# Kernel optimization log

Measured on AMD Instinct MI355X. Metric: run time of the kernel, lower is better.

Reference implementation:

```python
import jax, jax.numpy as jnp
import numpy as np

PRIOR_HOURS = 48.0
INIT_TIME = 0.0
K = 13  # nr_ref_time_points (time_space)
L = 200  # time steps (axis_2)
D = 64   # features (axis_3)
B = 64

REF_TIME = jnp.asarray(np.linspace(INIT_TIME, PRIOR_HOURS, K).reshape(K, 1, 1), dtype=jnp.float32)


def setup_inputs() -> dict:
    key = jax.random.key(0)
    ks = jax.random.split(key, 9)
    X = jax.random.normal(ks[0], (B, L, D), dtype=jnp.float32)
    T = jax.random.uniform(ks[1], (B, L, D), dtype=jnp.float32) * PRIOR_HOURS
    M = (jax.random.uniform(ks[2], (B, L, D)) > 0.5).astype(jnp.float32)
    DT = jax.random.uniform(ks[3], (B, L, D), dtype=jnp.float32)
    # trainable weights (keras random_normal initializer, stddev=0.05)
    alpha = jax.random.normal(ks[4], (K, 1, 1), dtype=jnp.float32) * 0.05
    w_v = jax.random.normal(ks[5], (K, L, D), dtype=jnp.float32) * 0.05
    w_t = jax.random.normal(ks[6], (K, L, D, 4), dtype=jnp.float32) * 0.05
    b_v = jax.random.normal(ks[7], (K, 1, D), dtype=jnp.float32) * 0.05
    b_t = jax.random.normal(ks[8], (K, L, D, 1), dtype=jnp.float32) * 0.05
    return {"X": X, "T": T, "M": M, "DT": DT, "alpha": alpha,
            "w_v": w_v, "w_t": w_t, "b_v": b_v, "b_t": b_t}


def reference(X, T, M, DT, alpha, w_v, w_t, b_v, b_t):
    # broadcast inputs over the K reference time points: [B,1,L,D] -> [B,K,L,D]
    dist = jnp.abs(T[:, None, :, :] - REF_TIME)                 # [B,K,L,D]
    kernel = jnp.exp(-jax.nn.relu(alpha) * dist)                # [B,K,L,D]
    intensity = jax.nn.relu(X[:, None, :, :] * kernel)          # [B,K,L,D]
    shp = intensity.shape
    x = jnp.broadcast_to(X[:, None, :, :], shp)
    dt = jnp.broadcast_to(DT[:, None, :, :], shp)
    m = jnp.broadcast_to(M[:, None, :, :], shp)
    feat = jnp.stack([x, dt, intensity, m], axis=-1)            # [B,K,L,D,4]
    # stage 1: weighted reduce over the 4-feature axis (b_t broadcasts over it)
    lat = jax.nn.relu(jnp.sum(w_t * feat + b_t, axis=-1))       # [B,K,L,D]
    # stage 2: weighted reduce over the time-step axis L (b_v broadcasts over it)
    out = jax.nn.relu(jnp.sum(w_v * lat + b_v, axis=2))         # [B,K,D]
    return out
```

## Files before the change

### kernel.cpp

```cpp
#include <hip/hip_runtime.h>


#define NB 64
#define NK 13
#define NL 200
#define ND 64
#define ND4 16
#define GB 8
#define LC 2
#define NC (NL / LC)

__global__ __launch_bounds__(256) void alnn_stage1(
    const float* __restrict__ X, const float* __restrict__ T,
    const float* __restrict__ M, const float* __restrict__ DT,
    const float* __restrict__ alpha, const float* __restrict__ w_v,
    const float* __restrict__ w_t, const float* __restrict__ b_t,
    float4* __restrict__ part)
{
    const int bid = blockIdx.x;
    const int clo = bid & 7;
    const int g   = bid >> 3;
    const int bg  = g & 7;
    const int chi = g >> 3;
    const int c   = chi * 8 + clo;
    if (c >= NC) return;

    const int tid = threadIdx.x;
    const int dq  = tid & 15;
    const int b8  = (tid >> 4) & 7;
    const int ks  = tid >> 7;
    const int k0  = ks * 7;
    const int b   = (bg << 3) + b8;
    const int la  = c * LC;

    const float4* X4  = (const float4*)X;
    const float4* T4  = (const float4*)T;
    const float4* M4  = (const float4*)M;
    const float4* DT4 = (const float4*)DT;
    const float4* WT4 = (const float4*)w_t;
    const float4* BT4 = (const float4*)b_t;
    const float4* WV4 = (const float4*)w_v;

    float av[7], rv[7];
    #pragma unroll
    for (int i = 0; i < 7; ++i) {
        const int k = k0 + i;
        av[i] = (k < NK) ? fmaxf(alpha[k], 0.f) : 0.f;
        rv[i] = 4.f * (float)k;
    }

    float4 acc[7];
    #pragma unroll
    for (int i = 0; i < 7; ++i) acc[i] = make_float4(0.f, 0.f, 0.f, 0.f);

#define COMP(c_, wt, A) {                                                 \
        const float dist  = fabsf(t4.c_ - reft);                          \
        const float inten = fmaxf(x4.c_ * __expf(-a * dist), 0.f);        \
        const float sf = wt.x * x4.c_ + wt.y * dt4.c_ + wt.z * inten +    \
                         wt.w * m4.c_ + 4.f * bt4.c_;                     \
        A.c_ = fmaf(wv4.c_, fmaxf(sf, 0.f), A.c_);                        \
    }

    #pragma unroll
    for (int li = 0; li < LC; ++li) {
        const int l  = la + li;
        const int io = (b * NL + l) * ND4 + dq;
        const float4 x4  = X4[io];
        const float4 t4  = T4[io];
        const float4 m4  = M4[io];
        const float4 dt4 = DT4[io];
        #pragma unroll
        for (int i = 0; i < 7; ++i) {
            const int k = k0 + i;
            if (k < NK) {
                const int w0 = (k * NL + l) * ND + (dq << 2);
                const float4 wt0 = WT4[w0 + 0];
                const float4 wt1 = WT4[w0 + 1];
                const float4 wt2 = WT4[w0 + 2];
                const float4 wt3 = WT4[w0 + 3];
                const int   wq  = (k * NL + l) * ND4 + dq;
                const float4 bt4 = BT4[wq];
                const float4 wv4 = WV4[wq];
                const float a    = av[i];
                const float reft = rv[i];
                COMP(x, wt0, acc[i])
                COMP(y, wt1, acc[i])
                COMP(z, wt2, acc[i])
                COMP(w, wt3, acc[i])
            }
        }
    }
#undef COMP

    const int pb = ((c * NB + b) * NK + k0) * ND4 + dq;
    #pragma unroll
    for (int i = 0; i < 7; ++i)
        if (k0 + i < NK) part[pb + i * ND4] = acc[i];
}

__global__ __launch_bounds__(256) void alnn_stage2(
    const float4* __restrict__ part, const float* __restrict__ b_v,
    float4* __restrict__ out)
{
    const int g  = blockIdx.x * 256 + threadIdx.x;
    const int dq = g & 15;
    const int r  = g >> 4;
    const int q  = r & 3;
    const int bk = r >> 2;
    if (bk >= NB * NK) return;

    float4 s = make_float4(0.f, 0.f, 0.f, 0.f);
    #pragma unroll 5
    for (int i = 0; i < NC / 4; ++i) {
        const int c = q * (NC / 4) + i;
        const float4 p = part[(c * NB * NK + bk) * ND4 + dq];
        s.x += p.x; s.y += p.y; s.z += p.z; s.w += p.w;
    }
    s.x += __shfl_xor(s.x, 16); s.y += __shfl_xor(s.y, 16);
    s.z += __shfl_xor(s.z, 16); s.w += __shfl_xor(s.w, 16);
    s.x += __shfl_xor(s.x, 32); s.y += __shfl_xor(s.y, 32);
    s.z += __shfl_xor(s.z, 32); s.w += __shfl_xor(s.w, 32);

    if (q == 0) {
        const int k = bk % NK;
        const float4 bv = ((const float4*)b_v)[k * ND4 + dq];
        float4 o;
        o.x = fmaxf(s.x + 200.f * bv.x, 0.f);
        o.y = fmaxf(s.y + 200.f * bv.y, 0.f);
        o.z = fmaxf(s.z + 200.f * bv.z, 0.f);
        o.w = fmaxf(s.w + 200.f * bv.w, 0.f);
        out[bk * ND4 + dq] = o;
    }
}

extern "C" void kernel_launch(void* const* d_in, const int* in_sizes, int n_in,
                              void* d_out, int out_size, void* d_ws, size_t ws_size,
                              hipStream_t stream) {
    const float* X     = (const float*)d_in[0];
    const float* T     = (const float*)d_in[1];
    const float* M     = (const float*)d_in[2];
    const float* DT    = (const float*)d_in[3];
    const float* alpha = (const float*)d_in[4];
    const float* w_v   = (const float*)d_in[5];
    const float* w_t   = (const float*)d_in[6];
    const float* b_v   = (const float*)d_in[7];
    const float* b_t   = (const float*)d_in[8];

    float4* part = (float4*)d_ws;

    alnn_stage1<<<832, 256, 0, stream>>>(X, T, M, DT, alpha, w_v, w_t, b_t, part);
    alnn_stage2<<<(NB * NK * 64) / 256, 256, 0, stream>>>(part, b_v, (float4*)d_out);
}
```

Before: 101.4 us.

## Split L chunk across thread halves and pre-reduce partials with shuffles

Each stage-1 block now covers 4 time steps, with the two 16-lane halves of a 32-lane group each taking two. The K split moves from threads to blocks. Partials are combined with an xor-16 shuffle before being stored, and writes are split between the halves. This halves the number of partial chunks, which cuts workspace traffic and stage-2 reduction work. Stage 2 reads the chunks with an interleaved stride instead. The cost is fewer threads per (b,k) pair, extra shuffles, and one more block for the ragged tail.

```diff
diff --git a/kernel.cpp b/kernel.cpp
--- a/kernel.cpp
+++ b/kernel.cpp
@@ -6,8 +6,7 @@
 #define NL 200
 #define ND 64
 #define ND4 16
-#define GB 8
-#define LC 2
+#define LC 4
 #define NC (NL / LC)
 
 __global__ __launch_bounds__(256) void alnn_stage1(
@@ -20,18 +19,19 @@
     const int bid = blockIdx.x;
     const int clo = bid & 7;
     const int g   = bid >> 3;
-    const int bg  = g & 7;
-    const int chi = g >> 3;
+    const int ks  = g & 1;
+    const int bg  = (g >> 1) & 7;
+    const int chi = g >> 4;
     const int c   = chi * 8 + clo;
     if (c >= NC) return;
 
     const int tid = threadIdx.x;
     const int dq  = tid & 15;
-    const int b8  = (tid >> 4) & 7;
-    const int ks  = tid >> 7;
+    const int lh  = (tid >> 4) & 1;
+    const int b8  = tid >> 5;
     const int k0  = ks * 7;
     const int b   = (bg << 3) + b8;
-    const int la  = c * LC;
+    const int la  = c * LC + (lh << 1);
 
     const float4* X4  = (const float4*)X;
     const float4* T4  = (const float4*)T;
@@ -62,7 +62,7 @@
     }
 
     #pragma unroll
-    for (int li = 0; li < LC; ++li) {
+    for (int li = 0; li < 2; ++li) {
         const int l  = la + li;
         const int io = (b * NL + l) * ND4 + dq;
         const float4 x4  = X4[io];
@@ -92,10 +92,21 @@
     }
 #undef COMP
 
+    #pragma unroll
+    for (int i = 0; i < 7; ++i) {
+        acc[i].x += __shfl_xor(acc[i].x, 16);
+        acc[i].y += __shfl_xor(acc[i].y, 16);
+        acc[i].z += __shfl_xor(acc[i].z, 16);
+        acc[i].w += __shfl_xor(acc[i].w, 16);
+    }
+
     const int pb = ((c * NB + b) * NK + k0) * ND4 + dq;
     #pragma unroll
-    for (int i = 0; i < 7; ++i)
-        if (k0 + i < NK) part[pb + i * ND4] = acc[i];
+    for (int i = 0; i < 7; ++i) {
+        const int k = k0 + i;
+        if (k < NK && ((i < 4) == (lh == 0)))
+            part[pb + i * ND4] = acc[i];
+    }
 }
 
 __global__ __launch_bounds__(256) void alnn_stage2(
@@ -110,11 +121,13 @@
     if (bk >= NB * NK) return;
 
     float4 s = make_float4(0.f, 0.f, 0.f, 0.f);
-    #pragma unroll 5
-    for (int i = 0; i < NC / 4; ++i) {
-        const int c = q * (NC / 4) + i;
-        const float4 p = part[(c * NB * NK + bk) * ND4 + dq];
-        s.x += p.x; s.y += p.y; s.z += p.z; s.w += p.w;
+    #pragma unroll
+    for (int i = 0; i < 13; ++i) {
+        const int c = q + (i << 2);
+        if (c < NC) {
+            const float4 p = part[(c * NB * NK + bk) * ND4 + dq];
+            s.x += p.x; s.y += p.y; s.z += p.z; s.w += p.w;
+        }
     }
     s.x += __shfl_xor(s.x, 16); s.y += __shfl_xor(s.y, 16);
     s.z += __shfl_xor(s.z, 16); s.w += __shfl_xor(s.w, 16);
@@ -148,6 +161,6 @@
 
     float4* part = (float4*)d_ws;
 
-    alnn_stage1<<<832, 256, 0, stream>>>(X, T, M, DT, alpha, w_v, w_t, b_t, part);
+    alnn_stage1<<<896, 256, 0, stream>>>(X, T, M, DT, alpha, w_v, w_t, b_t, part);
     alnn_stage2<<<(NB * NK * 64) / 256, 256, 0, stream>>>(part, b_v, (float4*)d_out);
 }
```

Result: slower. 112.2 us (+10.6%).
